# Kernel optimization log

Hardware: AMD Instinct MI355X
Metric: run time of the kernel (lower is better)

Reference implementation:

```python
import jax, jax.numpy as jnp
import numpy as np

E = 8      # n_rm_states
D = 256    # flattened input dim
H = 64     # hidden width (hard-coded in module)
A = 18     # n_actions
B = 65536  # batch


def setup_inputs() -> dict:
    key = jax.random.key(0)
    ks = jax.random.split(key, 16)
    s = lambda k, shape, fan_in: jax.random.normal(k, shape, jnp.float32) * (1.0 / np.sqrt(fan_in))
    inp = {
        "state": jax.random.normal(ks[0], (B, D), jnp.float32),
        "rm_state": jax.random.randint(ks[1], (B,), 0, E),
        # stacked per-expert params: layer i weight [E, in, out], bias [E, out]
        "W1": s(ks[2], (E, D, H), D), "b1": jnp.zeros((E, H), jnp.float32),
        "W2": s(ks[3], (E, H, H), H), "b2": jnp.zeros((E, H), jnp.float32),
        "W3": s(ks[4], (E, H, H), H), "b3": jnp.zeros((E, H), jnp.float32),
        "W4": s(ks[5], (E, H, H), H), "b4": jnp.zeros((E, H), jnp.float32),
        "W5": s(ks[6], (E, H, H), H), "b5": jnp.zeros((E, H), jnp.float32),
        "W6": s(ks[7], (E, H, A), H), "b6": jnp.zeros((E, A), jnp.float32),
    }
    return inp


def reference(state, rm_state, W1, b1, W2, b2, W3, b3, W4, b4, W5, b5, W6, b6):
    x = state.reshape(state.shape[0], -1)              # [B, D]
    # Run all E expert MLPs densely over the batch, then select per-row expert.
    h = jax.nn.relu(jnp.einsum('bd,edh->ebh', x, W1) + b1[:, None, :])   # [E, B, H]
    h = jax.nn.relu(jnp.einsum('ebh,ehk->ebk', h, W2) + b2[:, None, :])
    h = jax.nn.relu(jnp.einsum('ebh,ehk->ebk', h, W3) + b3[:, None, :])
    h = jax.nn.relu(jnp.einsum('ebh,ehk->ebk', h, W4) + b4[:, None, :])
    h = jax.nn.relu(jnp.einsum('ebh,ehk->ebk', h, W5) + b5[:, None, :])
    out_all = jnp.einsum('ebh,eha->eba', h, W6) + b6[:, None, :]          # [E, B, A]
    # scatter-back: actions[b] = expert[rm_state[b]](x[b])
    actions = out_all[rm_state, jnp.arange(x.shape[0])]                    # [B, A]
    return actions
```

## Files before the change

kernel.cpp:

```cpp
#include <hip/hip_runtime.h>
#include <hip/hip_bf16.h>


#define NE   8
#define DIM  256
#define HID  64
#define NA   18

typedef __attribute__((ext_vector_type(8))) short short8;
typedef __attribute__((ext_vector_type(4))) float f32x4;
#define MFMA __builtin_amdgcn_mfma_f32_16x16x32_bf16

__device__ __forceinline__ unsigned short f2bf(float f) {
    unsigned u = __builtin_bit_cast(unsigned, f);
    u += 0x7fff + ((u >> 16) & 1);
    return (unsigned short)(u >> 16);
}
__device__ __forceinline__ float bf2f(unsigned short h) {
    unsigned u = ((unsigned)h) << 16;
    return __builtin_bit_cast(float, u);
}
__device__ __forceinline__ void split8v(const float* xs, short8& hi, short8& lo) {
    float back[8];
    #pragma unroll
    for (int p = 0; p < 4; ++p) {
        __hip_bfloat162 h2 = __float22bfloat162_rn(make_float2(xs[2*p], xs[2*p+1]));
        hi[2*p]   = (short)__builtin_bit_cast(unsigned short, h2.x);
        hi[2*p+1] = (short)__builtin_bit_cast(unsigned short, h2.y);
        float2 b2 = __bfloat1622float2(h2);
        back[2*p] = b2.x; back[2*p+1] = b2.y;
    }
    #pragma unroll
    for (int p = 0; p < 4; ++p) {
        __hip_bfloat162 l2 = __float22bfloat162_rn(
            make_float2(xs[2*p] - back[2*p], xs[2*p+1] - back[2*p+1]));
        lo[2*p]   = (short)__builtin_bit_cast(unsigned short, l2.x);
        lo[2*p+1] = (short)__builtin_bit_cast(unsigned short, l2.y);
    }
}

__global__ __launch_bounds__(256) void prep_histo(
    const float* __restrict__ W1, const float* __restrict__ W2,
    const float* __restrict__ W3, const float* __restrict__ W4,
    const float* __restrict__ W5, const float* __restrict__ W6,
    short* __restrict__ W1H, short* __restrict__ W1L,
    short* __restrict__ W2H, short* __restrict__ W2L,
    short* __restrict__ W3H, short* __restrict__ W3L,
    short* __restrict__ W4H, short* __restrict__ W4L,
    short* __restrict__ W5H, short* __restrict__ W5L,
    short* __restrict__ W6H, short* __restrict__ W6L,
    const int* __restrict__ rm, int* __restrict__ hist) {
    const int bid = blockIdx.x;
    if (bid >= 1088) {
        __shared__ int wch[4][NE];
        const int blk = bid - 1088;
        const int t = threadIdx.x, w = t >> 6, l = t & 63;
        const int e = rm[blk * 256 + t];
        #pragma unroll
        for (int q = 0; q < NE; ++q) {
            unsigned long long m = __ballot(e == q);
            if (l == 0) wch[w][q] = __popcll(m);
        }
        __syncthreads();
        if (t < NE) hist[blk * NE + t] = wch[0][t] + wch[1][t] + wch[2][t] + wch[3][t];
        return;
    }
    const int idx = bid * 256 + threadIdx.x;
    float v; short* H; short* L; int sidx;
    if (idx < 131072) {
        int e = idx >> 14, r = idx & 16383;
        int ks = r >> 11, nt = (r >> 9) & 3, l = (r >> 3) & 63, j = r & 7;
        int k = ks * 32 + ((l >> 4) << 3) + j, n = (nt << 4) + (l & 15);
        v = W1[(e * DIM + k) * HID + n];
        H = W1H; L = W1L; sidx = idx;
    } else if (idx < 131072 + 4 * 32768) {
        int layer = (idx - 131072) >> 15;
        int local = (idx - 131072) & 32767;
        int e = local >> 12, r = local & 4095;
        int ks = r >> 11, nt = (r >> 9) & 3, l = (r >> 3) & 63, j = r & 7;
        int k = ks * 32 + ((l >> 4) << 3) + j, n = (nt << 4) + (l & 15);
        const float* W = (layer == 0) ? W2 : (layer == 1) ? W3 : (layer == 2) ? W4 : W5;
        v = W[(e * HID + k) * HID + n];
        H = (layer == 0) ? W2H : (layer == 1) ? W3H : (layer == 2) ? W4H : W5H;
        L = (layer == 0) ? W2L : (layer == 1) ? W3L : (layer == 2) ? W4L : W5L;
        sidx = local;
    } else {
        int local = idx - (131072 + 4 * 32768);
        int e = local >> 11, r = local & 2047;
        int ks = r >> 10, nt = (r >> 9) & 1, l = (r >> 3) & 63, j = r & 7;
        int k = ks * 32 + ((l >> 4) << 3) + j, n = (nt << 4) + (l & 15);
        v = (n < NA) ? W6[(e * HID + k) * NA + n] : 0.0f;
        H = W6H; L = W6L; sidx = local;
    }
    unsigned short h = f2bf(v);
    H[sidx] = (short)h;
    L[sidx] = (short)f2bf(v - bf2f(h));
}

__global__ __launch_bounds__(512) void scan_scatter(const int* __restrict__ rm,
                                                    const int* __restrict__ hist,
                                                    int* __restrict__ perm,
                                                    int* __restrict__ meta) {
    __shared__ int sbuf[NE][256];
    __shared__ int wc[8][NE];
    __shared__ int wb2[4][NE];
    __shared__ int baseE[NE];
    const int t = threadIdx.x, w = t >> 6, l = t & 63;
    const int myblk = blockIdx.x;

    {
        int v0 = hist[(l * 4 + 0) * NE + w];
        int v1 = hist[(l * 4 + 1) * NE + w];
        int v2 = hist[(l * 4 + 2) * NE + w];
        int v3 = hist[(l * 4 + 3) * NE + w];
        v1 += v0; v2 += v1; v3 += v2;
        int s = v3;
        #pragma unroll
        for (int off = 1; off < 64; off <<= 1) {
            int u = __shfl_up(s, off);
            if (l >= off) s += u;
        }
        const int ex = s - v3;
        sbuf[w][l * 4 + 0] = ex + v0;
        sbuf[w][l * 4 + 1] = ex + v1;
        sbuf[w][l * 4 + 2] = ex + v2;
        sbuf[w][l * 4 + 3] = ex + v3;
    }
    __syncthreads();
    if (t < NE) {
        int es = 0;
        for (int q = 0; q < t; ++q) es += sbuf[q][255];
        baseE[t] = es + (myblk ? sbuf[t][myblk - 1] : 0);
    }
    if (myblk == 0 && t == 0) {
        int es = 0, ts = 0;
        meta[8] = 0; meta[17] = 0;
        for (int e = 0; e < NE; ++e) {
            int c = sbuf[e][255];
            meta[e] = c;
            es += c; meta[8 + e + 1] = es;
            ts += (c + 63) >> 6; meta[17 + e + 1] = ts;
        }
    }
    const int i = myblk * 256 + t;
    const int e_row = (t < 256) ? rm[i] : -1;
    const unsigned long long ltm = (1ull << l) - 1ull;
    int rank = 0;
    #pragma unroll
    for (int q = 0; q < NE; ++q) {
        unsigned long long m = __ballot(e_row == q);
        if (e_row == q) rank = __popcll(m & ltm);
        if (l == 0) wc[w][q] = __popcll(m);
    }
    __syncthreads();
    if (t < 32) {
        int ww = t >> 3, q = t & 7;
        int b = baseE[q];
        for (int p = 0; p < ww; ++p) b += wc[p][q];
        wb2[ww][q] = b;
    }
    __syncthreads();
    if (t < 256) perm[wb2[w][e_row] + rank] = i;
}

template <int NT>
__device__ __forceinline__ void gemm_k64(const float* hsrc, int l,
                                         const short* __restrict__ WH,
                                         const short* __restrict__ WL,
                                         f32x4* a0, f32x4* a1, f32x4* a2) {
    const int lg = l >> 4, lr = l & 15;
    #pragma unroll
    for (int ks = 0; ks < 2; ++ks) {
        const float* ap = hsrc + lr * 68 + ks * 32 + lg * 8;
        float4 v0 = *(const float4*)(ap);
        float4 v1 = *(const float4*)(ap + 4);
        float xs[8] = {v0.x, v0.y, v0.z, v0.w, v1.x, v1.y, v1.z, v1.w};
        short8 ahi, alo; split8v(xs, ahi, alo);
        short8 bh[NT], bl[NT];
        #pragma unroll
        for (int nt = 0; nt < NT; ++nt) {
            bh[nt] = *(const short8*)(WH + ((ks * NT + nt) * 64 + l) * 8);
            bl[nt] = *(const short8*)(WL + ((ks * NT + nt) * 64 + l) * 8);
        }
        #pragma unroll
        for (int nt = 0; nt < NT; ++nt) {
            a0[nt] = MFMA(ahi, bh[nt], a0[nt], 0, 0, 0);
            a1[nt] = MFMA(alo, bh[nt], a1[nt], 0, 0, 0);
            a2[nt] = MFMA(ahi, bl[nt], a2[nt], 0, 0, 0);
        }
    }
}

template <int NT, bool RELU>
__device__ __forceinline__ void finish_to_lds(float* hdst, int l,
                                              const float* __restrict__ bias,
                                              f32x4* a0, f32x4* a1, f32x4* a2) {
    const int lg = l >> 4, lr = l & 15;
    #pragma unroll
    for (int nt = 0; nt < NT; ++nt) {
        float bv = bias[nt * 16 + lr];
        #pragma unroll
        for (int r = 0; r < 4; ++r) {
            float v = (a0[nt][r] + a1[nt][r]) + (a2[nt][r] + bv);
            if (RELU) v = fmaxf(v, 0.0f);
            hdst[(lg * 4 + r) * 68 + nt * 16 + lr] = v;
        }
    }
}

__global__ __launch_bounds__(256, 4) void mlp_mfma(
    const float* __restrict__ x, const int* __restrict__ perm,
    const int* __restrict__ meta,
    const short* __restrict__ W1H, const short* __restrict__ W1L,
    const short* __restrict__ W2H, const short* __restrict__ W2L,
    const short* __restrict__ W3H, const short* __restrict__ W3L,
    const short* __restrict__ W4H, const short* __restrict__ W4L,
    const short* __restrict__ W5H, const short* __restrict__ W5L,
    const short* __restrict__ W6H, const short* __restrict__ W6L,
    const float* __restrict__ b1, const float* __restrict__ b2,
    const float* __restrict__ b3, const float* __restrict__ b4,
    const float* __restrict__ b5, const float* __restrict__ b6,
    float* __restrict__ out) {
    __shared__ __align__(16) float hbuf[4][16][68];
    const int blk = blockIdx.x;
    if (blk >= meta[17 + NE]) return;
    int e = 0;
    #pragma unroll 1
    while (blk >= meta[17 + e + 1]) ++e;
    const int lt = blk - meta[17 + e];
    const int cnt = meta[e];
    const int pbase = meta[8 + e];
    const int t = threadIdx.x, w = t >> 6, l = t & 63;
    const int lg = l >> 4, lr = l & 15;
    const int li = lt * 64 + w * 16 + lr;
    const int row = perm[pbase + min(li, cnt - 1)];
    float* hw = &hbuf[w][0][0];
    const f32x4 zero = {0.0f, 0.0f, 0.0f, 0.0f};

    {
        f32x4 a0[4] = {zero, zero, zero, zero};
        f32x4 a1[4] = {zero, zero, zero, zero};
        f32x4 a2[4] = {zero, zero, zero, zero};
        const float* xr = x + (size_t)row * DIM + lg * 8;
        const short* WHp = W1H + (size_t)e * 32 * 512 + l * 8;
        const short* WLp = W1L + (size_t)e * 32 * 512 + l * 8;
        #pragma unroll
        for (int ks = 0; ks < 8; ++ks) {
            float4 v0 = *(const float4*)(xr + ks * 32);
            float4 v1 = *(const float4*)(xr + ks * 32 + 4);
            float xs[8] = {v0.x, v0.y, v0.z, v0.w, v1.x, v1.y, v1.z, v1.w};
            short8 ahi, alo; split8v(xs, ahi, alo);
            short8 bh[4], bl[4];
            #pragma unroll
            for (int nt = 0; nt < 4; ++nt) {
                bh[nt] = *(const short8*)(WHp + (ks * 4 + nt) * 512);
                bl[nt] = *(const short8*)(WLp + (ks * 4 + nt) * 512);
            }
            #pragma unroll
            for (int nt = 0; nt < 4; ++nt) {
                a0[nt] = MFMA(ahi, bh[nt], a0[nt], 0, 0, 0);
                a1[nt] = MFMA(alo, bh[nt], a1[nt], 0, 0, 0);
                a2[nt] = MFMA(ahi, bl[nt], a2[nt], 0, 0, 0);
            }
        }
        finish_to_lds<4, true>(hw, l, b1 + e * HID, a0, a1, a2);
    }
    #define HIDDEN(WH_, WL_, bias_)                                   \
    {                                                                 \
        f32x4 a0[4] = {zero, zero, zero, zero};                       \
        f32x4 a1[4] = {zero, zero, zero, zero};                       \
        f32x4 a2[4] = {zero, zero, zero, zero};                       \
        gemm_k64<4>(hw, l, WH_ + e * 8 * 512, WL_ + e * 8 * 512,      \
                    a0, a1, a2);                                      \
        finish_to_lds<4, true>(hw, l, bias_ + e * HID, a0, a1, a2);   \
    }
    HIDDEN(W2H, W2L, b2)
    HIDDEN(W3H, W3L, b3)
    HIDDEN(W4H, W4L, b4)
    HIDDEN(W5H, W5L, b5)
    #undef HIDDEN
    {
        f32x4 a0[2] = {zero, zero};
        f32x4 a1[2] = {zero, zero};
        f32x4 a2[2] = {zero, zero};
        gemm_k64<2>(hw, l, W6H + e * 4 * 512, W6L + e * 4 * 512, a0, a1, a2);
        const float* b6p = b6 + e * NA;
        #pragma unroll
        for (int r = 0; r < 4; ++r) {
            const int drow = lg * 4 + r;
            const int rs = __shfl(row, drow, 64);
            const bool valid = (lt * 64 + w * 16 + drow) < cnt;
            #pragma unroll
            for (int nt = 0; nt < 2; ++nt) {
                const int col = nt * 16 + lr;
                if (valid && col < NA)
                    out[(size_t)rs * NA + col] = (a0[nt][r] + a1[nt][r]) + (a2[nt][r] + b6p[col]);
            }
        }
    }
}

extern "C" void kernel_launch(void* const* d_in, const int* in_sizes, int n_in,
                              void* d_out, int out_size, void* d_ws, size_t ws_size,
                              hipStream_t stream) {
    const float* x  = (const float*)d_in[0];
    const int*   rm = (const int*)d_in[1];
    const float* W1 = (const float*)d_in[2];   const float* b1 = (const float*)d_in[3];
    const float* W2 = (const float*)d_in[4];   const float* b2 = (const float*)d_in[5];
    const float* W3 = (const float*)d_in[6];   const float* b3 = (const float*)d_in[7];
    const float* W4 = (const float*)d_in[8];   const float* b4 = (const float*)d_in[9];
    const float* W5 = (const float*)d_in[10];  const float* b5 = (const float*)d_in[11];
    const float* W6 = (const float*)d_in[12];  const float* b6 = (const float*)d_in[13];
    float* out = (float*)d_out;

    const int B = in_sizes[1];
    const int nblk = B / 256;

    int* hist = (int*)d_ws;
    int* meta = hist + nblk * NE;
    int* perm = meta + 32;
    short* W1H = (short*)(perm + B);
    short* W1L = W1H + 131072;
    short* W2H = W1L + 131072;  short* W2L = W2H + 32768;
    short* W3H = W2L + 32768;   short* W3L = W3H + 32768;
    short* W4H = W3L + 32768;   short* W4L = W4H + 32768;
    short* W5H = W4L + 32768;   short* W5L = W5H + 32768;
    short* W6H = W5L + 32768;   short* W6L = W6H + 16384;

    prep_histo<<<1088 + nblk, 256, 0, stream>>>(W1, W2, W3, W4, W5, W6,
                                                W1H, W1L, W2H, W2L, W3H, W3L,
                                                W4H, W4L, W5H, W5L, W6H, W6L,
                                                rm, hist);
    scan_scatter<<<nblk, 512, 0, stream>>>(rm, hist, perm, meta);
    mlp_mfma<<<B / 64 + NE, 256, 0, stream>>>(x, perm, meta,
                                              W1H, W1L, W2H, W2L, W3H, W3L,
                                              W4H, W4L, W5H, W5L, W6H, W6L,
                                              b1, b2, b3, b4, b5, b6, out);
}
```

Baseline: 148.4 us.

## Process two 16-row M-tiles per wave and vectorize weight prep stores

Each wave in the main MLP kernel now handles 32 rows (two 16-row MFMA tiles) instead of 16, so every B-fragment load of the hi/lo weight splits is reused across two tiles. The block tile grows to 128 rows, with tile counts and grid size changed to match, and launch bounds drop from 4 to 2 waves per SIMD to make room for the doubled accumulators. Separately, the weight split prep kernel now has each thread convert 8 consecutive K values and write a short8 vector, cutting its block count by 8x. The cost is higher register and LDS use per block and fewer blocks to spread across CUs.

Result: slower. 155.2 us (+4.5%).

```diff
diff --git a/kernel.cpp b/kernel.cpp
--- a/kernel.cpp
+++ b/kernel.cpp
@@ -51,9 +51,9 @@
     short* __restrict__ W6H, short* __restrict__ W6L,
     const int* __restrict__ rm, int* __restrict__ hist) {
     const int bid = blockIdx.x;
-    if (bid >= 1088) {
+    if (bid >= 136) {
         __shared__ int wch[4][NE];
-        const int blk = bid - 1088;
+        const int blk = bid - 136;
         const int t = threadIdx.x, w = t >> 6, l = t & 63;
         const int e = rm[blk * 256 + t];
         #pragma unroll
@@ -65,36 +65,47 @@
         if (t < NE) hist[blk * NE + t] = wch[0][t] + wch[1][t] + wch[2][t] + wch[3][t];
         return;
     }
-    const int idx = bid * 256 + threadIdx.x;
-    float v; short* H; short* L; int sidx;
-    if (idx < 131072) {
-        int e = idx >> 14, r = idx & 16383;
-        int ks = r >> 11, nt = (r >> 9) & 3, l = (r >> 3) & 63, j = r & 7;
-        int k = ks * 32 + ((l >> 4) << 3) + j, n = (nt << 4) + (l & 15);
-        v = W1[(e * DIM + k) * HID + n];
-        H = W1H; L = W1L; sidx = idx;
-    } else if (idx < 131072 + 4 * 32768) {
-        int layer = (idx - 131072) >> 15;
-        int local = (idx - 131072) & 32767;
-        int e = local >> 12, r = local & 4095;
-        int ks = r >> 11, nt = (r >> 9) & 3, l = (r >> 3) & 63, j = r & 7;
-        int k = ks * 32 + ((l >> 4) << 3) + j, n = (nt << 4) + (l & 15);
+    const int u = bid * 256 + threadIdx.x;
+    const float* src; int sstride, dbase, n, npad;
+    short *H, *L;
+    if (u < 16384) {
+        int e = u >> 11, r = u & 2047;
+        int ks = r >> 8, nt = (r >> 6) & 3, l = r & 63;
+        int k0 = ks * 32 + ((l >> 4) << 3); n = (nt << 4) + (l & 15);
+        src = W1 + ((size_t)(e * DIM + k0)) * HID + n;
+        sstride = HID; npad = HID;
+        H = W1H; L = W1L; dbase = e * 16384 + ((ks * 4 + nt) * 64 + l) * 8;
+    } else if (u < 32768) {
+        int u2 = u - 16384;
+        int layer = u2 >> 12, local = u2 & 4095;
+        int e = local >> 9, r = local & 511;
+        int ks = r >> 8, nt = (r >> 6) & 3, l = r & 63;
+        int k0 = ks * 32 + ((l >> 4) << 3); n = (nt << 4) + (l & 15);
         const float* W = (layer == 0) ? W2 : (layer == 1) ? W3 : (layer == 2) ? W4 : W5;
-        v = W[(e * HID + k) * HID + n];
+        src = W + ((size_t)(e * HID + k0)) * HID + n;
+        sstride = HID; npad = HID;
         H = (layer == 0) ? W2H : (layer == 1) ? W3H : (layer == 2) ? W4H : W5H;
         L = (layer == 0) ? W2L : (layer == 1) ? W3L : (layer == 2) ? W4L : W5L;
-        sidx = local;
+        dbase = e * 4096 + ((ks * 4 + nt) * 64 + l) * 8;
     } else {
-        int local = idx - (131072 + 4 * 32768);
-        int e = local >> 11, r = local & 2047;
-        int ks = r >> 10, nt = (r >> 9) & 1, l = (r >> 3) & 63, j = r & 7;
-        int k = ks * 32 + ((l >> 4) << 3) + j, n = (nt << 4) + (l & 15);
-        v = (n < NA) ? W6[(e * HID + k) * NA + n] : 0.0f;
-        H = W6H; L = W6L; sidx = local;
-    }
-    unsigned short h = f2bf(v);
-    H[sidx] = (short)h;
-    L[sidx] = (short)f2bf(v - bf2f(h));
+        int u3 = u - 32768;
+        int e = u3 >> 8, r = u3 & 255;
+        int ks = r >> 7, nt = (r >> 6) & 1, l = r & 63;
+        int k0 = ks * 32 + ((l >> 4) << 3); n = (nt << 4) + (l & 15);
+        src = W6 + ((size_t)(e * HID + k0)) * NA + n;
+        sstride = NA; npad = NA;
+        H = W6H; L = W6L; dbase = e * 2048 + ((ks * 2 + nt) * 64 + l) * 8;
+    }
+    short8 hs, ls;
+    #pragma unroll
+    for (int j = 0; j < 8; ++j) {
+        float v = (n < npad) ? src[j * sstride] : 0.0f;
+        unsigned short h = f2bf(v);
+        hs[j] = (short)h;
+        ls[j] = (short)f2bf(v - bf2f(h));
+    }
+    *(short8*)(H + dbase) = hs;
+    *(short8*)(L + dbase) = ls;
 }
 
 __global__ __launch_bounds__(512) void scan_scatter(const int* __restrict__ rm,
@@ -139,7 +150,7 @@
             int c = sbuf[e][255];
             meta[e] = c;
             es += c; meta[8 + e + 1] = es;
-            ts += (c + 63) >> 6; meta[17 + e + 1] = ts;
+            ts += (c + 127) >> 7; meta[17 + e + 1] = ts;
         }
     }
     const int i = myblk * 256 + t;
@@ -164,18 +175,25 @@
 }
 
 template <int NT>
-__device__ __forceinline__ void gemm_k64(const float* hsrc, int l,
-                                         const short* __restrict__ WH,
-                                         const short* __restrict__ WL,
-                                         f32x4* a0, f32x4* a1, f32x4* a2) {
+__device__ __forceinline__ void gemm2_k64(const float* h0, const float* h1, int l,
+                                          const short* __restrict__ WH,
+                                          const short* __restrict__ WL,
+                                          f32x4 (*a0)[NT], f32x4 (*a1)[NT],
+                                          f32x4 (*a2)[NT]) {
     const int lg = l >> 4, lr = l & 15;
     #pragma unroll
     for (int ks = 0; ks < 2; ++ks) {
-        const float* ap = hsrc + lr * 68 + ks * 32 + lg * 8;
-        float4 v0 = *(const float4*)(ap);
-        float4 v1 = *(const float4*)(ap + 4);
-        float xs[8] = {v0.x, v0.y, v0.z, v0.w, v1.x, v1.y, v1.z, v1.w};
-        short8 ahi, alo; split8v(xs, ahi, alo);
+        const float* ap0 = h0 + lr * 68 + ks * 32 + lg * 8;
+        const float* ap1 = h1 + lr * 68 + ks * 32 + lg * 8;
+        float4 u0 = *(const float4*)(ap0);
+        float4 u1 = *(const float4*)(ap0 + 4);
+        float4 v0 = *(const float4*)(ap1);
+        float4 v1 = *(const float4*)(ap1 + 4);
+        float xs0[8] = {u0.x, u0.y, u0.z, u0.w, u1.x, u1.y, u1.z, u1.w};
+        float xs1[8] = {v0.x, v0.y, v0.z, v0.w, v1.x, v1.y, v1.z, v1.w};
+        short8 ahi0, alo0, ahi1, alo1;
+        split8v(xs0, ahi0, alo0);
+        split8v(xs1, ahi1, alo1);
         short8 bh[NT], bl[NT];
         #pragma unroll
         for (int nt = 0; nt < NT; ++nt) {
@@ -184,31 +202,37 @@
         }
         #pragma unroll
         for (int nt = 0; nt < NT; ++nt) {
-            a0[nt] = MFMA(ahi, bh[nt], a0[nt], 0, 0, 0);
-            a1[nt] = MFMA(alo, bh[nt], a1[nt], 0, 0, 0);
-            a2[nt] = MFMA(ahi, bl[nt], a2[nt], 0, 0, 0);
+            a0[0][nt] = MFMA(ahi0, bh[nt], a0[0][nt], 0, 0, 0);
+            a0[1][nt] = MFMA(ahi1, bh[nt], a0[1][nt], 0, 0, 0);
+            a1[0][nt] = MFMA(alo0, bh[nt], a1[0][nt], 0, 0, 0);
+            a1[1][nt] = MFMA(alo1, bh[nt], a1[1][nt], 0, 0, 0);
+            a2[0][nt] = MFMA(ahi0, bl[nt], a2[0][nt], 0, 0, 0);
+            a2[1][nt] = MFMA(ahi1, bl[nt], a2[1][nt], 0, 0, 0);
         }
     }
 }
 
 template <int NT, bool RELU>
-__device__ __forceinline__ void finish_to_lds(float* hdst, int l,
-                                              const float* __restrict__ bias,
-                                              f32x4* a0, f32x4* a1, f32x4* a2) {
+__device__ __forceinline__ void finish2(float* h0, float* h1, int l,
+                                        const float* __restrict__ bias,
+                                        f32x4 (*a0)[NT], f32x4 (*a1)[NT],
+                                        f32x4 (*a2)[NT]) {
     const int lg = l >> 4, lr = l & 15;
     #pragma unroll
     for (int nt = 0; nt < NT; ++nt) {
         float bv = bias[nt * 16 + lr];
         #pragma unroll
         for (int r = 0; r < 4; ++r) {
-            float v = (a0[nt][r] + a1[nt][r]) + (a2[nt][r] + bv);
-            if (RELU) v = fmaxf(v, 0.0f);
-            hdst[(lg * 4 + r) * 68 + nt * 16 + lr] = v;
-        }
-    }
-}
-
-__global__ __launch_bounds__(256, 4) void mlp_mfma(
+            float v0 = (a0[0][nt][r] + a1[0][nt][r]) + (a2[0][nt][r] + bv);
+            float v1 = (a0[1][nt][r] + a1[1][nt][r]) + (a2[1][nt][r] + bv);
+            if (RELU) { v0 = fmaxf(v0, 0.0f); v1 = fmaxf(v1, 0.0f); }
+            h0[(lg * 4 + r) * 68 + nt * 16 + lr] = v0;
+            h1[(lg * 4 + r) * 68 + nt * 16 + lr] = v1;
+        }
+    }
+}
+
+__global__ __launch_bounds__(256, 2) void mlp_mfma(
     const float* __restrict__ x, const int* __restrict__ perm,
     const int* __restrict__ meta,
     const short* __restrict__ W1H, const short* __restrict__ W1L,
@@ -221,7 +245,7 @@
     const float* __restrict__ b3, const float* __restrict__ b4,
     const float* __restrict__ b5, const float* __restrict__ b6,
     float* __restrict__ out) {
-    __shared__ __align__(16) float hbuf[4][16][68];
+    __shared__ __align__(16) float hbuf[4][2][16][68];
     const int blk = blockIdx.x;
     if (blk >= meta[17 + NE]) return;
     int e = 0;
@@ -232,24 +256,35 @@
     const int pbase = meta[8 + e];
     const int t = threadIdx.x, w = t >> 6, l = t & 63;
     const int lg = l >> 4, lr = l & 15;
-    const int li = lt * 64 + w * 16 + lr;
-    const int row = perm[pbase + min(li, cnt - 1)];
-    float* hw = &hbuf[w][0][0];
+    const int li0 = lt * 128 + w * 32 + lr;
+    const int li1 = li0 + 16;
+    const int row0 = perm[pbase + min(li0, cnt - 1)];
+    const int row1 = perm[pbase + min(li1, cnt - 1)];
+    float* h0 = &hbuf[w][0][0][0];
+    float* h1 = &hbuf[w][1][0][0];
     const f32x4 zero = {0.0f, 0.0f, 0.0f, 0.0f};
 
     {
-        f32x4 a0[4] = {zero, zero, zero, zero};
-        f32x4 a1[4] = {zero, zero, zero, zero};
-        f32x4 a2[4] = {zero, zero, zero, zero};
-        const float* xr = x + (size_t)row * DIM + lg * 8;
-        const short* WHp = W1H + (size_t)e * 32 * 512 + l * 8;
-        const short* WLp = W1L + (size_t)e * 32 * 512 + l * 8;
+        f32x4 a0[2][4], a1[2][4], a2[2][4];
+        #pragma unroll
+        for (int m = 0; m < 2; ++m)
+            #pragma unroll
+            for (int nt = 0; nt < 4; ++nt) { a0[m][nt] = zero; a1[m][nt] = zero; a2[m][nt] = zero; }
+        const float* xr0 = x + (size_t)row0 * DIM + lg * 8;
+        const float* xr1 = x + (size_t)row1 * DIM + lg * 8;
+        const short* WHp = W1H + (size_t)e * 16384 + l * 8;
+        const short* WLp = W1L + (size_t)e * 16384 + l * 8;
         #pragma unroll
         for (int ks = 0; ks < 8; ++ks) {
-            float4 v0 = *(const float4*)(xr + ks * 32);
-            float4 v1 = *(const float4*)(xr + ks * 32 + 4);
-            float xs[8] = {v0.x, v0.y, v0.z, v0.w, v1.x, v1.y, v1.z, v1.w};
-            short8 ahi, alo; split8v(xs, ahi, alo);
+            float4 u0 = *(const float4*)(xr0 + ks * 32);
+            float4 u1 = *(const float4*)(xr0 + ks * 32 + 4);
+            float4 v0 = *(const float4*)(xr1 + ks * 32);
+            float4 v1 = *(const float4*)(xr1 + ks * 32 + 4);
+            float xs0[8] = {u0.x, u0.y, u0.z, u0.w, u1.x, u1.y, u1.z, u1.w};
+            float xs1[8] = {v0.x, v0.y, v0.z, v0.w, v1.x, v1.y, v1.z, v1.w};
+            short8 ahi0, alo0, ahi1, alo1;
+            split8v(xs0, ahi0, alo0);
+            split8v(xs1, ahi1, alo1);
             short8 bh[4], bl[4];
             #pragma unroll
             for (int nt = 0; nt < 4; ++nt) {
@@ -258,21 +293,25 @@
             }
             #pragma unroll
             for (int nt = 0; nt < 4; ++nt) {
-                a0[nt] = MFMA(ahi, bh[nt], a0[nt], 0, 0, 0);
-                a1[nt] = MFMA(alo, bh[nt], a1[nt], 0, 0, 0);
-                a2[nt] = MFMA(ahi, bl[nt], a2[nt], 0, 0, 0);
+                a0[0][nt] = MFMA(ahi0, bh[nt], a0[0][nt], 0, 0, 0);
+                a0[1][nt] = MFMA(ahi1, bh[nt], a0[1][nt], 0, 0, 0);
+                a1[0][nt] = MFMA(alo0, bh[nt], a1[0][nt], 0, 0, 0);
+                a1[1][nt] = MFMA(alo1, bh[nt], a1[1][nt], 0, 0, 0);
+                a2[0][nt] = MFMA(ahi0, bl[nt], a2[0][nt], 0, 0, 0);
+                a2[1][nt] = MFMA(ahi1, bl[nt], a2[1][nt], 0, 0, 0);
             }
         }
-        finish_to_lds<4, true>(hw, l, b1 + e * HID, a0, a1, a2);
-    }
-    #define HIDDEN(WH_, WL_, bias_)                                   \
-    {                                                                 \
-        f32x4 a0[4] = {zero, zero, zero, zero};                       \
-        f32x4 a1[4] = {zero, zero, zero, zero};                       \
-        f32x4 a2[4] = {zero, zero, zero, zero};                       \
-        gemm_k64<4>(hw, l, WH_ + e * 8 * 512, WL_ + e * 8 * 512,      \
-                    a0, a1, a2);                                      \
-        finish_to_lds<4, true>(hw, l, bias_ + e * HID, a0, a1, a2);   \
+        finish2<4, true>(h0, h1, l, b1 + e * HID, a0, a1, a2);
+    }
+    #define HIDDEN(WH_, WL_, bias_)                                         \
+    {                                                                       \
+        f32x4 a0[2][4], a1[2][4], a2[2][4];                                 \
+        _Pragma("unroll")                                                   \
+        for (int m = 0; m < 2; ++m)                                         \
+            _Pragma("unroll")                                               \
+            for (int nt = 0; nt < 4; ++nt) { a0[m][nt] = zero; a1[m][nt] = zero; a2[m][nt] = zero; } \
+        gemm2_k64<4>(h0, h1, l, WH_ + e * 4096, WL_ + e * 4096, a0, a1, a2);\
+        finish2<4, true>(h0, h1, l, bias_ + e * HID, a0, a1, a2);           \
     }
     HIDDEN(W2H, W2L, b2)
     HIDDEN(W3H, W3L, b3)
@@ -280,21 +319,28 @@
     HIDDEN(W5H, W5L, b5)
     #undef HIDDEN
     {
-        f32x4 a0[2] = {zero, zero};
-        f32x4 a1[2] = {zero, zero};
-        f32x4 a2[2] = {zero, zero};
-        gemm_k64<2>(hw, l, W6H + e * 4 * 512, W6L + e * 4 * 512, a0, a1, a2);
+        f32x4 a0[2][2], a1[2][2], a2[2][2];
+        #pragma unroll
+        for (int m = 0; m < 2; ++m)
+            #pragma unroll
+            for (int nt = 0; nt < 2; ++nt) { a0[m][nt] = zero; a1[m][nt] = zero; a2[m][nt] = zero; }
+        gemm2_k64<2>(h0, h1, l, W6H + e * 2048, W6L + e * 2048, a0, a1, a2);
         const float* b6p = b6 + e * NA;
         #pragma unroll
-        for (int r = 0; r < 4; ++r) {
-            const int drow = lg * 4 + r;
-            const int rs = __shfl(row, drow, 64);
-            const bool valid = (lt * 64 + w * 16 + drow) < cnt;
-            #pragma unroll
-            for (int nt = 0; nt < 2; ++nt) {
-                const int col = nt * 16 + lr;
-                if (valid && col < NA)
-                    out[(size_t)rs * NA + col] = (a0[nt][r] + a1[nt][r]) + (a2[nt][r] + b6p[col]);
+        for (int m = 0; m < 2; ++m) {
+            const int rowm = m ? row1 : row0;
+            #pragma unroll
+            for (int r = 0; r < 4; ++r) {
+                const int drow = lg * 4 + r;
+                const int rs = __shfl(rowm, drow, 64);
+                const bool valid = (lt * 128 + w * 32 + m * 16 + drow) < cnt;
+                #pragma unroll
+                for (int nt = 0; nt < 2; ++nt) {
+                    const int col = nt * 16 + lr;
+                    if (valid && col < NA)
+                        out[(size_t)rs * NA + col] =
+                            (a0[m][nt][r] + a1[m][nt][r]) + (a2[m][nt][r] + b6p[col]);
+                }
             }
         }
     }
@@ -327,13 +373,13 @@
     short* W5H = W4L + 32768;   short* W5L = W5H + 32768;
     short* W6H = W5L + 32768;   short* W6L = W6H + 16384;
 
-    prep_histo<<<1088 + nblk, 256, 0, stream>>>(W1, W2, W3, W4, W5, W6,
-                                                W1H, W1L, W2H, W2L, W3H, W3L,
-                                                W4H, W4L, W5H, W5L, W6H, W6L,
-                                                rm, hist);
+    prep_histo<<<136 + nblk, 256, 0, stream>>>(W1, W2, W3, W4, W5, W6,
+                                               W1H, W1L, W2H, W2L, W3H, W3L,
+                                               W4H, W4L, W5H, W5L, W6H, W6L,
+                                               rm, hist);
     scan_scatter<<<nblk, 512, 0, stream>>>(rm, hist, perm, meta);
-    mlp_mfma<<<B / 64 + NE, 256, 0, stream>>>(x, perm, meta,
-                                              W1H, W1L, W2H, W2L, W3H, W3L,
-                                              W4H, W4L, W5H, W5L, W6H, W6L,
-                                              b1, b2, b3, b4, b5, b6, out);
-}
+    mlp_mfma<<<B / 128 + NE, 256, 0, stream>>>(x, perm, meta,
+                                               W1H, W1L, W2H, W2L, W3H, W3L,
+                                               W4H, W4L, W5H, W5L, W6H, W6L,
+                                               b1, b2, b3, b4, b5, b6, out);
+}
```
